# Kernel tuning notes

Hardware: AMD Instinct MI355X
Metric: run time of the kernel (lower is better)

The kernel has to match this reference:

```python
import jax, jax.numpy as jnp
import numpy as np

EPS = 1e-06


def setup_inputs() -> dict:
    key = jax.random.key(0)
    k1, k2 = jax.random.split(key)
    N, C, H, W = 256, 3, 256, 256
    preds = jax.random.normal(k1, (N, C, H, W), dtype=jnp.float32)
    targets = jax.random.normal(k2, (N, C, H, W), dtype=jnp.float32)
    return {"preds": preds, "targets": targets}


def reference(preds, targets):
    N = preds.shape[0]
    # Flatten to [N, D] as in torch's .view(len, -1)
    Z = targets.reshape(N, -1)  # targets first, matching the torch call order
    B = preds.reshape(N, -1)
    Z_c = Z - jnp.mean(Z, axis=1, keepdims=True)
    B_c = B - jnp.mean(B, axis=1, keepdims=True)
    # Full N x N cross-correlation matrix (faithful to original), then diagonal
    num = jnp.einsum('nd,md->nm', Z_c, B_c)
    Z_norm = jnp.linalg.norm(Z_c, axis=1, keepdims=True)  # [N,1]
    B_norm = jnp.linalg.norm(B_c, axis=1, keepdims=True)  # [N,1]
    denom = Z_norm @ B_norm.T  # [N,N]
    pearson = num / (denom + EPS)
    corr = jnp.diagonal(pearson)  # [N]
    return jnp.mean(corr)  # reduction='mean'
```

## Files before the change

### kernel.cpp

```cpp
#include <hip/hip_runtime.h>
#include <stdint.h>


typedef float f4 __attribute__((ext_vector_type(4)));

constexpr int NROWS  = 256;
constexpr int D      = 3 * 256 * 256;
constexpr int D4     = D / 4;
constexpr int TPB1   = 256;
constexpr int BATCH  = 4;
constexpr int C4     = TPB1 * BATCH;
constexpr int CHUNKS = D4 / C4;
constexpr double EPS = 1e-6;

__device__ __forceinline__ void async_ld16(const void* g, void* l) {
    __builtin_amdgcn_global_load_lds(
        (const __attribute__((address_space(1))) uint32_t*)g,
        (__attribute__((address_space(3))) uint32_t*)l,
        16, 0, 2);
}

__global__ __launch_bounds__(TPB1) void partial_kernel(
        const f4* __restrict__ preds,
        const f4* __restrict__ targets,
        double* __restrict__ partials)
{
    __shared__ f4 sBuf[2][BATCH][TPB1];

    const int  blk   = blockIdx.x;
    const int  row   = blk / CHUNKS;
    const int  chunk = blk % CHUNKS;
    const int  tid   = threadIdx.x;
    const int  w     = tid >> 6;
    const long G     = (long)row * D4 + (long)chunk * C4;

    #pragma unroll
    for (int u = 0; u < BATCH; ++u) {
        const long gi = G + (long)u * TPB1 + tid;
        async_ld16(&preds[gi],   &sBuf[0][u][w * 64]);
        async_ld16(&targets[gi], &sBuf[1][u][w * 64]);
    }
    __syncthreads();

    double sZ = 0.0, sB = 0.0, sZZ = 0.0, sBB = 0.0, sZB = 0.0;
    #pragma unroll
    for (int u = 0; u < BATCH; ++u) {
        const f4 b4 = sBuf[0][u][tid];
        const f4 z4 = sBuf[1][u][tid];
        double z, b;
        z = (double)z4.x; b = (double)b4.x;
        sZ += z; sB += b; sZZ = fma(z,z,sZZ); sBB = fma(b,b,sBB); sZB = fma(z,b,sZB);
        z = (double)z4.y; b = (double)b4.y;
        sZ += z; sB += b; sZZ = fma(z,z,sZZ); sBB = fma(b,b,sBB); sZB = fma(z,b,sZB);
        z = (double)z4.z; b = (double)b4.z;
        sZ += z; sB += b; sZZ = fma(z,z,sZZ); sBB = fma(b,b,sBB); sZB = fma(z,b,sZB);
        z = (double)z4.w; b = (double)b4.w;
        sZ += z; sB += b; sZZ = fma(z,z,sZZ); sBB = fma(b,b,sBB); sZB = fma(z,b,sZB);
    }

    #pragma unroll
    for (int off = 32; off > 0; off >>= 1) {
        sZ  += __shfl_down(sZ,  off);
        sB  += __shfl_down(sB,  off);
        sZZ += __shfl_down(sZZ, off);
        sBB += __shfl_down(sBB, off);
        sZB += __shfl_down(sZB, off);
    }

    constexpr int NWAVES = TPB1 / 64;
    __shared__ double sm[5][NWAVES];
    const int lane = tid & 63;
    if (lane == 0) {
        sm[0][w] = sZ;  sm[1][w] = sB;
        sm[2][w] = sZZ; sm[3][w] = sBB;
        sm[4][w] = sZB;
    }
    __syncthreads();

    if (tid == 0) {
        double* out = partials + (long)blk * 5;
        #pragma unroll
        for (int k = 0; k < 5; ++k)
            out[k] = sm[k][0] + sm[k][1] + sm[k][2] + sm[k][3];
    }
}

__global__ __launch_bounds__(64) void row_reduce_kernel(
        const double* __restrict__ partials, double* __restrict__ rowcorr)
{
    const int row = blockIdx.x;
    const int c   = threadIdx.x;
    double tZ = 0, tB = 0, tZZ = 0, tBB = 0, tZB = 0;
    if (c < CHUNKS) {
        const double* p = partials + ((long)row * CHUNKS + c) * 5;
        tZ = p[0]; tB = p[1]; tZZ = p[2]; tBB = p[3]; tZB = p[4];
    }
    #pragma unroll
    for (int off = 32; off > 0; off >>= 1) {
        tZ  += __shfl_down(tZ,  off);
        tB  += __shfl_down(tB,  off);
        tZZ += __shfl_down(tZZ, off);
        tBB += __shfl_down(tBB, off);
        tZB += __shfl_down(tZB, off);
    }
    if (c == 0) {
        const double invD = 1.0 / (double)D;
        const double num  = tZB - tZ * tB * invD;
        const double varZ = fmax(tZZ - tZ * tZ * invD, 0.0);
        const double varB = fmax(tBB - tB * tB * invD, 0.0);
        const double den  = sqrt(varZ) * sqrt(varB) + EPS;
        rowcorr[row] = num / den;
    }
}

__global__ __launch_bounds__(NROWS) void mean_kernel(
        const double* __restrict__ rowcorr, float* __restrict__ out)
{
    const int tid = threadIdx.x;
    double v = rowcorr[tid];
    #pragma unroll
    for (int off = 32; off > 0; off >>= 1) v += __shfl_down(v, off);

    __shared__ double sm[NROWS / 64];
    const int wave = tid >> 6;
    const int lane = tid & 63;
    if (lane == 0) sm[wave] = v;
    __syncthreads();
    if (tid == 0) {
        double t = 0.0;
        #pragma unroll
        for (int w = 0; w < NROWS / 64; ++w) t += sm[w];
        out[0] = (float)(t / (double)NROWS);
    }
}

extern "C" void kernel_launch(void* const* d_in, const int* in_sizes, int n_in,
                              void* d_out, int out_size, void* d_ws, size_t ws_size,
                              hipStream_t stream) {
    const f4* preds   = (const f4*)d_in[0];
    const f4* targets = (const f4*)d_in[1];
    double* partials = (double*)d_ws;
    double* rowcorr  = partials + (long)NROWS * CHUNKS * 5;
    float*  out      = (float*)d_out;

    hipLaunchKernelGGL(partial_kernel, dim3(NROWS * CHUNKS), dim3(TPB1), 0, stream,
                       preds, targets, partials);
    hipLaunchKernelGGL(row_reduce_kernel, dim3(NROWS), dim3(64), 0, stream,
                       partials, rowcorr);
    hipLaunchKernelGGL(mean_kernel, dim3(1), dim3(NROWS), 0, stream,
                       rowcorr, out);
}
```

Measured before the change: 358.5 us.

## Make partial kernel persistent per-wave with double-buffered async LDS loads

Replaces the one-shot blocks (one chunk per block, 12288 blocks) with 512 blocks in which each wave streams one eighth of a row. Loads go through a two-stage async global-to-LDS pipeline with explicit vmcnt waits, so the next stage's loads overlap the FP64 accumulation of the current one. Each wave writes its own partial sums, and the row-reduce and mean kernels are merged into a single finalize kernel, saving one launch. The fixed grid may leave some compute units underused, and the hand-written waitcnt counts must match the number of outstanding loads exactly. There is also a leftover dead loop in finalize.

```diff
diff --git a/kernel.cpp b/kernel.cpp
--- a/kernel.cpp
+++ b/kernel.cpp
@@ -4,14 +4,18 @@
 
 typedef float f4 __attribute__((ext_vector_type(4)));
 
-constexpr int NROWS  = 256;
-constexpr int D      = 3 * 256 * 256;
-constexpr int D4     = D / 4;
-constexpr int TPB1   = 256;
-constexpr int BATCH  = 4;
-constexpr int C4     = TPB1 * BATCH;
-constexpr int CHUNKS = D4 / C4;
-constexpr double EPS = 1e-6;
+constexpr int    NROWS    = 256;
+constexpr int    D        = 3 * 256 * 256;
+constexpr int    D4       = D / 4;
+constexpr int    TPB      = 256;
+constexpr int    WPB      = TPB / 64;
+constexpr int    WPR      = 8;
+constexpr int    NBLOCKS  = NROWS * WPR / WPB;
+constexpr int    K        = 4;
+constexpr int    STAGE_F4 = 64 * K;
+constexpr int    WAVE_F4  = D4 / WPR;
+constexpr int    NSTAGES  = WAVE_F4 / STAGE_F4;
+constexpr double EPS      = 1e-6;
 
 __device__ __forceinline__ void async_ld16(const void* g, void* l) {
     __builtin_amdgcn_global_load_lds(
@@ -20,42 +24,77 @@
         16, 0, 2);
 }
 
-__global__ __launch_bounds__(TPB1) void partial_kernel(
+__global__ __launch_bounds__(TPB, 2) void partial_kernel(
         const f4* __restrict__ preds,
         const f4* __restrict__ targets,
         double* __restrict__ partials)
 {
-    __shared__ f4 sBuf[2][BATCH][TPB1];
+    __shared__ f4 sBuf[WPB][2][2][K][64];
 
-    const int  blk   = blockIdx.x;
-    const int  row   = blk / CHUNKS;
-    const int  chunk = blk % CHUNKS;
-    const int  tid   = threadIdx.x;
-    const int  w     = tid >> 6;
-    const long G     = (long)row * D4 + (long)chunk * C4;
+    const int  tid  = threadIdx.x;
+    const int  w    = tid >> 6;
+    const int  lane = tid & 63;
+    const int  gw   = blockIdx.x * WPB + w;
+    const int  row  = gw >> 3;
+    const int  seg  = gw & (WPR - 1);
+    const long gbase = (long)row * D4 + (long)seg * WAVE_F4;
 
-    #pragma unroll
-    for (int u = 0; u < BATCH; ++u) {
-        const long gi = G + (long)u * TPB1 + tid;
-        async_ld16(&preds[gi],   &sBuf[0][u][w * 64]);
-        async_ld16(&targets[gi], &sBuf[1][u][w * 64]);
+    auto issue = [&](int t, int p) {
+        const long gb = gbase + (long)t * STAGE_F4;
+        #pragma unroll
+        for (int u = 0; u < K; ++u) {
+            async_ld16(&preds[gb + u * 64 + lane],   &sBuf[w][p][0][u][0]);
+            async_ld16(&targets[gb + u * 64 + lane], &sBuf[w][p][1][u][0]);
+        }
+    };
+
+    issue(0, 0);
+    issue(1, 1);
+
+    double sZ = 0, sB = 0, sZZ = 0, sBB = 0, sZB = 0;
+
+    auto accum = [&](const f4* bv, const f4* zv) {
+        #pragma unroll
+        for (int u = 0; u < K; ++u) {
+            #pragma unroll
+            for (int c = 0; c < 4; ++c) {
+                const double b = (double)bv[u][c];
+                const double z = (double)zv[u][c];
+                sZ += z; sB += b;
+                sZZ = fma(z, z, sZZ);
+                sBB = fma(b, b, sBB);
+                sZB = fma(z, b, sZB);
+            }
+        }
+    };
+
+    for (int t = 0; t < NSTAGES - 1; ++t) {
+        const int p = t & 1;
+        asm volatile("s_waitcnt vmcnt(8)" ::: "memory");
+        __builtin_amdgcn_sched_barrier(0);
+        f4 bv[K], zv[K];
+        #pragma unroll
+        for (int u = 0; u < K; ++u) {
+            bv[u] = sBuf[w][p][0][u][lane];
+            zv[u] = sBuf[w][p][1][u][lane];
+        }
+        asm volatile("s_waitcnt lgkmcnt(0)" ::: "memory");
+        __builtin_amdgcn_sched_barrier(0);
+        if (t + 2 < NSTAGES) issue(t + 2, p);
+        accum(bv, zv);
     }
-    __syncthreads();
-
-    double sZ = 0.0, sB = 0.0, sZZ = 0.0, sBB = 0.0, sZB = 0.0;
-    #pragma unroll
-    for (int u = 0; u < BATCH; ++u) {
-        const f4 b4 = sBuf[0][u][tid];
-        const f4 z4 = sBuf[1][u][tid];
-        double z, b;
-        z = (double)z4.x; b = (double)b4.x;
-        sZ += z; sB += b; sZZ = fma(z,z,sZZ); sBB = fma(b,b,sBB); sZB = fma(z,b,sZB);
-        z = (double)z4.y; b = (double)b4.y;
-        sZ += z; sB += b; sZZ = fma(z,z,sZZ); sBB = fma(b,b,sBB); sZB = fma(z,b,sZB);
-        z = (double)z4.z; b = (double)b4.z;
-        sZ += z; sB += b; sZZ = fma(z,z,sZZ); sBB = fma(b,b,sBB); sZB = fma(z,b,sZB);
-        z = (double)z4.w; b = (double)b4.w;
-        sZ += z; sB += b; sZZ = fma(z,z,sZZ); sBB = fma(b,b,sBB); sZB = fma(z,b,sZB);
+    {
+        const int p = (NSTAGES - 1) & 1;
+        asm volatile("s_waitcnt vmcnt(0)" ::: "memory");
+        __builtin_amdgcn_sched_barrier(0);
+        f4 bv[K], zv[K];
+        #pragma unroll
+        for (int u = 0; u < K; ++u) {
+            bv[u] = sBuf[w][p][0][u][lane];
+            zv[u] = sBuf[w][p][1][u][lane];
+        }
+        asm volatile("s_waitcnt lgkmcnt(0)" ::: "memory");
+        accum(bv, zv);
     }
 
     #pragma unroll
@@ -66,70 +105,50 @@
         sBB += __shfl_down(sBB, off);
         sZB += __shfl_down(sZB, off);
     }
-
-    constexpr int NWAVES = TPB1 / 64;
-    __shared__ double sm[5][NWAVES];
-    const int lane = tid & 63;
     if (lane == 0) {
-        sm[0][w] = sZ;  sm[1][w] = sB;
-        sm[2][w] = sZZ; sm[3][w] = sBB;
-        sm[4][w] = sZB;
-    }
-    __syncthreads();
-
-    if (tid == 0) {
-        double* out = partials + (long)blk * 5;
-        #pragma unroll
-        for (int k = 0; k < 5; ++k)
-            out[k] = sm[k][0] + sm[k][1] + sm[k][2] + sm[k][3];
+        double* o = partials + (long)gw * 5;
+        o[0] = sZ; o[1] = sB; o[2] = sZZ; o[3] = sBB; o[4] = sZB;
     }
 }
 
-__global__ __launch_bounds__(64) void row_reduce_kernel(
-        const double* __restrict__ partials, double* __restrict__ rowcorr)
+__global__ __launch_bounds__(NROWS) void finalize_kernel(
+        const double* __restrict__ partials, float* __restrict__ out)
 {
-    const int row = blockIdx.x;
-    const int c   = threadIdx.x;
+    const int r = threadIdx.x;
+    const double* p = partials + (long)r * WPR * 5;
     double tZ = 0, tB = 0, tZZ = 0, tBB = 0, tZB = 0;
-    if (c < CHUNKS) {
-        const double* p = partials + ((long)row * CHUNKS + c) * 5;
-        tZ = p[0]; tB = p[1]; tZZ = p[2]; tBB = p[3]; tZB = p[4];
+    #pragma unroll
+    for (int s = 0; s < WPR; ++s) {
+        tB  += p[s * 5 + 1 - 1 + 0];
     }
+    tZ = 0; tB = 0; tZZ = 0; tBB = 0; tZB = 0;
     #pragma unroll
-    for (int off = 32; off > 0; off >>= 1) {
-        tZ  += __shfl_down(tZ,  off);
-        tB  += __shfl_down(tB,  off);
-        tZZ += __shfl_down(tZZ, off);
-        tBB += __shfl_down(tBB, off);
-        tZB += __shfl_down(tZB, off);
+    for (int s = 0; s < WPR; ++s) {
+        tZ  += p[s * 5 + 0];
+        tB  += p[s * 5 + 1];
+        tZZ += p[s * 5 + 2];
+        tBB += p[s * 5 + 3];
+        tZB += p[s * 5 + 4];
     }
-    if (c == 0) {
-        const double invD = 1.0 / (double)D;
-        const double num  = tZB - tZ * tB * invD;
-        const double varZ = fmax(tZZ - tZ * tZ * invD, 0.0);
-        const double varB = fmax(tBB - tB * tB * invD, 0.0);
-        const double den  = sqrt(varZ) * sqrt(varB) + EPS;
-        rowcorr[row] = num / den;
-    }
-}
+    const double invD = 1.0 / (double)D;
+    const double num  = tZB - tZ * tB * invD;
+    const double varZ = fmax(tZZ - tZ * tZ * invD, 0.0);
+    const double varB = fmax(tBB - tB * tB * invD, 0.0);
+    const double den  = sqrt(varZ) * sqrt(varB) + EPS;
+    double corr = num / den;
 
-__global__ __launch_bounds__(NROWS) void mean_kernel(
-        const double* __restrict__ rowcorr, float* __restrict__ out)
-{
-    const int tid = threadIdx.x;
-    double v = rowcorr[tid];
     #pragma unroll
-    for (int off = 32; off > 0; off >>= 1) v += __shfl_down(v, off);
+    for (int off = 32; off > 0; off >>= 1) corr += __shfl_down(corr, off);
 
     __shared__ double sm[NROWS / 64];
-    const int wave = tid >> 6;
-    const int lane = tid & 63;
-    if (lane == 0) sm[wave] = v;
+    const int wave = r >> 6;
+    const int lane = r & 63;
+    if (lane == 0) sm[wave] = corr;
     __syncthreads();
-    if (tid == 0) {
+    if (r == 0) {
         double t = 0.0;
         #pragma unroll
-        for (int w = 0; w < NROWS / 64; ++w) t += sm[w];
+        for (int v = 0; v < NROWS / 64; ++v) t += sm[v];
         out[0] = (float)(t / (double)NROWS);
     }
 }
@@ -139,14 +158,11 @@
                               hipStream_t stream) {
     const f4* preds   = (const f4*)d_in[0];
     const f4* targets = (const f4*)d_in[1];
-    double* partials = (double*)d_ws;
-    double* rowcorr  = partials + (long)NROWS * CHUNKS * 5;
-    float*  out      = (float*)d_out;
+    double* partials  = (double*)d_ws;
+    float*  out       = (float*)d_out;
 
-    hipLaunchKernelGGL(partial_kernel, dim3(NROWS * CHUNKS), dim3(TPB1), 0, stream,
+    hipLaunchKernelGGL(partial_kernel, dim3(NBLOCKS), dim3(TPB), 0, stream,
                        preds, targets, partials);
-    hipLaunchKernelGGL(row_reduce_kernel, dim3(NROWS), dim3(64), 0, stream,
-                       partials, rowcorr);
-    hipLaunchKernelGGL(mean_kernel, dim3(1), dim3(NROWS), 0, stream,
-                       rowcorr, out);
+    hipLaunchKernelGGL(finalize_kernel, dim3(1), dim3(NROWS), 0, stream,
+                       partials, out);
 }
```

Result: no change. 357.3 us (-0.3%).
